# Kernel tuning notes

Hardware: AMD Instinct MI355X
Metric: run time of the kernel (lower is better)

The kernel has to match this reference:

```python
import jax, jax.numpy as jnp
import numpy as np

B, C, N = 32, 512, 1024   # batch, input channels, tokens
E, D, H = 512, 2048, 8    # d_input, d_model, heads
T, O = 50, 1000           # iterations, out_dims
NA, NO = 512, 512         # n_synch_action, n_synch_out


def setup_inputs() -> dict:
    key = jax.random.key(0)
    ks = jax.random.split(key, 16)
    s = 0.02
    rn = lambda k, shape: jax.random.normal(k, shape, jnp.float32) * s
    return dict(
        x=jax.random.normal(ks[0], (B, C, N), jnp.float32),
        W_kv=rn(ks[1], (C, E)), b_kv=jnp.zeros(E), g_kv=jnp.ones(E), be_kv=jnp.zeros(E),
        W_q=rn(ks[2], (NA, E)), b_q=jnp.zeros(E),
        W_in=rn(ks[3], (E, 3 * E)), b_in=jnp.zeros(3 * E),
        W_ao=rn(ks[4], (E, E)), b_ao=jnp.zeros(E),
        W_syn=rn(ks[5], (E + D, 2 * D)), b_syn=jnp.zeros(2 * D),
        g_syn=jnp.ones(D), be_syn=jnp.zeros(D),
        g_pm=jnp.ones(D), be_pm=jnp.zeros(D),
        W1=rn(ks[6], (D, D)), b1=jnp.zeros(D),
        W2=rn(ks[7], (D, D)), b2=jnp.zeros(D),
        start_state=jax.random.uniform(ks[8], (D,), jnp.float32, -0.1, 0.1),
        decay_action=jnp.zeros(NA), decay_out=jnp.zeros(NO),
        W_out=rn(ks[9], (NO, O)), b_out=jnp.zeros(O),
        idx_action=jax.random.permutation(ks[10], D)[:NA].astype(jnp.int32),
        idx_out=jax.random.permutation(ks[11], D)[:NO].astype(jnp.int32),
    )


def _ln(x, g, b, eps=1e-5):
    m = x.mean(-1, keepdims=True)
    v = ((x - m) ** 2).mean(-1, keepdims=True)
    return (x - m) * jax.lax.rsqrt(v + eps) * g + b


def reference(x, W_kv, b_kv, g_kv, be_kv, W_q, b_q, W_in, b_in, W_ao, b_ao,
              W_syn, b_syn, g_syn, be_syn, g_pm, be_pm, W1, b1, W2, b2,
              start_state, decay_action, decay_out, W_out, b_out,
              idx_action, idx_out):
    Bx = x.shape[0]
    hd = E // H
    # features: backbone='none', pos='none' -> flatten(2).transpose(1,2) then kv_proj
    feats = jnp.transpose(x, (0, 2, 1))                 # [B,N,C]
    kv = _ln(feats @ W_kv + b_kv, g_kv, be_kv)          # [B,N,E]
    # MHA K/V are constant across iterations -> hoist
    Wq_a, Wk_a, Wv_a = jnp.split(W_in, 3, axis=1)
    bq_a, bk_a, bv_a = jnp.split(b_in, 3)
    K = (kv @ Wk_a + bk_a).reshape(Bx, N, H, hd)
    V = (kv @ Wv_a + bv_a).reshape(Bx, N, H, hd)
    r_a = jnp.exp(-jnp.clip(decay_action, 0.0, 15.0))   # [NA]
    r_o = jnp.exp(-jnp.clip(decay_out, 0.0, 15.0))      # [NO]
    act0 = jnp.broadcast_to(start_state, (Bx, D))
    zA = jnp.zeros((Bx, NA), jnp.float32)
    zO = jnp.zeros((Bx, NO), jnp.float32)
    logO = jnp.log(jnp.float32(O))
    scale = 1.0 / jnp.sqrt(jnp.float32(hd))

    def step(carry, _):
        act, aA, bA, aO, bO = carry
        # action sync (left == right in the source, so products are squares)
        sel = act[:, idx_action]
        aA = r_a * aA + sel * sel
        bA = r_a * bA + 1.0
        syncA = aA * jax.lax.rsqrt(bA)                  # [B,NA]
        # cross-attention query
        q = syncA @ W_q + b_q                           # [B,E]
        qh = (q @ Wq_a + bq_a).reshape(Bx, H, hd)
        scores = jnp.einsum('bhd,bnhd->bhn', qh, K) * scale
        w = jax.nn.softmax(scores, axis=-1)
        attn = jnp.einsum('bhn,bnhd->bhd', w, V).reshape(Bx, E)
        attn = attn @ W_ao + b_ao
        # synapses: LazyLinear(2D) -> GLU -> LayerNorm (dropout=0)
        h = jnp.concatenate([attn, act], axis=-1) @ W_syn + b_syn
        a_half, g_half = jnp.split(h, 2, axis=-1)
        state = _ln(a_half * jax.nn.sigmoid(g_half), g_syn, be_syn)
        # post-synapse MLP: LN -> Linear -> ReLU -> Linear -> ReLU
        hpm = _ln(state, g_pm, be_pm)
        act = jax.nn.relu(jax.nn.relu(hpm @ W1 + b1) @ W2 + b2)
        # out sync
        selo = act[:, idx_out]
        aO = r_o * aO + selo * selo
        bO = r_o * bO + 1.0
        syncO = aO * jax.lax.rsqrt(bO)                  # [B,NO]
        pred = syncO @ W_out + b_out                    # [B,O]
        lp = jax.nn.log_softmax(pred, axis=-1)
        ne = -jnp.sum(jnp.exp(lp) * lp, axis=-1) / logO
        cert = jnp.stack([ne, 1.0 - ne], axis=-1)       # [B,2]
        return (act, aA, bA, aO, bO), (pred, cert, syncO)

    _, (preds, certs, syncs) = jax.lax.scan(step, (act0, zA, zA, zO, zO), None, length=T)
    predictions = jnp.transpose(preds, (1, 2, 0))       # [B,O,T]
    certainties = jnp.transpose(certs, (1, 2, 0))       # [B,2,T]
    return predictions, certainties, syncs[-1]
```

## Files before the change

kernel.cpp:

```cpp
#include <hip/hip_runtime.h>


typedef unsigned short u16;
typedef unsigned int uv4 __attribute__((ext_vector_type(4)));
typedef float fv4 __attribute__((ext_vector_type(4)));
typedef float fv2 __attribute__((ext_vector_type(2)));

__device__ __forceinline__ float bf2f(u16 u) {
    return __uint_as_float(((unsigned int)u) << 16);
}
__device__ __forceinline__ float bflo(unsigned int u) { return __uint_as_float(u << 16); }
__device__ __forceinline__ float bfhi(unsigned int u) { return __uint_as_float(u & 0xffff0000u); }
__device__ __forceinline__ u16 f2bf(float f) {
    unsigned int u = __float_as_uint(f);
    unsigned int r = u + 0x7fffu + ((u >> 16) & 1u);
    return (u16)(r >> 16);
}

__device__ __forceinline__ void cload(fv4& r, const void* p) {
    asm volatile("global_load_dwordx4 %0, %1, off sc0 sc1" : "=v"(r) : "v"(p));
}
__device__ __forceinline__ void cload2(fv2& r, const void* p) {
    asm volatile("global_load_dwordx2 %0, %1, off sc0 sc1" : "=v"(r) : "v"(p));
}
__device__ __forceinline__ void cstore4(void* p, fv4 v) {
    asm volatile("global_store_dwordx4 %0, %1, off sc0 sc1" :: "v"(p), "v"(v) : "memory");
}
__device__ __forceinline__ void cstore2(void* p, fv2 v) {
    asm volatile("global_store_dwordx2 %0, %1, off sc0 sc1" :: "v"(p), "v"(v) : "memory");
}
__device__ __forceinline__ void cwait1(fv4& a) {
    asm volatile("s_waitcnt vmcnt(0)" : "+v"(a) :: "memory");
    __builtin_amdgcn_sched_barrier(0);
}
__device__ __forceinline__ void cwait2(fv4& a, fv4& b) {
    asm volatile("s_waitcnt vmcnt(0)" : "+v"(a), "+v"(b) :: "memory");
    __builtin_amdgcn_sched_barrier(0);
}
__device__ __forceinline__ void cwaitf2(fv2& a) {
    asm volatile("s_waitcnt vmcnt(0)" : "+v"(a) :: "memory");
    __builtin_amdgcn_sched_barrier(0);
}

__device__ __forceinline__ float aload(const float* p) {
    return __hip_atomic_load((const float*)p, __ATOMIC_RELAXED, __HIP_MEMORY_SCOPE_AGENT);
}

__global__ __launch_bounds__(256) void k_init(
    const float* __restrict__ start_state, const float* __restrict__ dec_a,
    const float* __restrict__ dec_o,
    float* act0, float* aA, float* bA, float* aO, float* bO,
    float* r_a, float* r_o, unsigned* bar)
{
    int g = blockIdx.x * 256 + threadIdx.x;
    int T = gridDim.x * 256;
    for (int i = g; i < 32 * 2048; i += T) act0[i] = start_state[i & 2047];
    for (int i = g; i < 32 * 512; i += T) { aA[i] = 0.f; bA[i] = 0.f; aO[i] = 0.f; bO[i] = 0.f; }
    for (int i = g; i < 512; i += T) {
        float da = fminf(fmaxf(dec_a[i], 0.f), 15.f);
        float dv = fminf(fmaxf(dec_o[i], 0.f), 15.f);
        r_a[i] = __expf(-da);
        r_o[i] = __expf(-dv);
    }
    if (g < 2048) bar[g] = 0u;
}

__global__ __launch_bounds__(256) void k_gemm_xT(
    const float* __restrict__ x, const float* __restrict__ Wkv,
    const float* __restrict__ bkv, float* __restrict__ out)
{
    __shared__ float As[16 * 68];
    __shared__ float Bs[16 * 132];
    int tid = threadIdx.x;
    int tn = tid & 15, tm = tid >> 4;
    int n0 = blockIdx.x * 128;
    int r0 = blockIdx.y * 64;
    int b = r0 >> 10;
    int nrow0 = r0 & 1023;
    const float* xb = x + (size_t)b * 512 * 1024;
    float acc[4][8];
#pragma unroll
    for (int i = 0; i < 4; ++i)
#pragma unroll
        for (int j = 0; j < 8; ++j) acc[i][j] = 0.f;

    for (int k0 = 0; k0 < 512; k0 += 16) {
        __syncthreads();
#pragma unroll
        for (int l = 0; l < 4; ++l) {
            int i = tid + l * 256;
            int nn = i & 63, kk = i >> 6;
            As[kk * 68 + nn] = xb[(size_t)(k0 + kk) * 1024 + nrow0 + nn];
        }
#pragma unroll
        for (int l = 0; l < 8; ++l) {
            int i = tid + l * 256;
            int n = i & 127, kk = i >> 7;
            Bs[kk * 132 + n] = Wkv[(size_t)(k0 + kk) * 512 + n0 + n];
        }
        __syncthreads();
#pragma unroll
        for (int k = 0; k < 16; ++k) {
            float4 a4 = *(const float4*)&As[k * 68 + tm * 4];
            float4 b0 = *(const float4*)&Bs[k * 132 + tn * 8];
            float4 b1 = *(const float4*)&Bs[k * 132 + tn * 8 + 4];
            float av[4] = {a4.x, a4.y, a4.z, a4.w};
            float bv[8] = {b0.x, b0.y, b0.z, b0.w, b1.x, b1.y, b1.z, b1.w};
#pragma unroll
            for (int i = 0; i < 4; ++i)
#pragma unroll
                for (int j = 0; j < 8; ++j) acc[i][j] += av[i] * bv[j];
        }
    }
#pragma unroll
    for (int i = 0; i < 4; ++i) {
        int r = r0 + tm * 4 + i;
        int c = n0 + tn * 8;
        float* orow = out + (size_t)r * 512 + c;
#pragma unroll
        for (int j = 0; j < 8; ++j) orow[j] = acc[i][j] + bkv[c + j];
    }
}

__global__ __launch_bounds__(256) void k_gemm_AB(
    const float* __restrict__ A, int lda,
    const float* __restrict__ B, int ldb,
    const float* __restrict__ bias,
    u16* __restrict__ out, int N)
{
    __shared__ float As[16 * 68];
    __shared__ float Bs[16 * 132];
    int tid = threadIdx.x;
    int tn = tid & 15, tm = tid >> 4;
    int n0 = blockIdx.x * 128;
    int r0 = blockIdx.y * 64;
    float acc[4][8];
#pragma unroll
    for (int i = 0; i < 4; ++i)
#pragma unroll
        for (int j = 0; j < 8; ++j) acc[i][j] = 0.f;

    for (int k0 = 0; k0 < 512; k0 += 16) {
        __syncthreads();
#pragma unroll
        for (int l = 0; l < 4; ++l) {
            int i = tid + l * 256;
            int kk = i & 15, m = i >> 4;
            As[kk * 68 + m] = A[(size_t)(r0 + m) * lda + k0 + kk];
        }
#pragma unroll
        for (int l = 0; l < 8; ++l) {
            int i = tid + l * 256;
            int n = i & 127, kk = i >> 7;
            Bs[kk * 132 + n] = B[(size_t)(k0 + kk) * ldb + n0 + n];
        }
        __syncthreads();
#pragma unroll
        for (int k = 0; k < 16; ++k) {
            float4 a4 = *(const float4*)&As[k * 68 + tm * 4];
            float4 b0 = *(const float4*)&Bs[k * 132 + tn * 8];
            float4 b1 = *(const float4*)&Bs[k * 132 + tn * 8 + 4];
            float av[4] = {a4.x, a4.y, a4.z, a4.w};
            float bv[8] = {b0.x, b0.y, b0.z, b0.w, b1.x, b1.y, b1.z, b1.w};
#pragma unroll
            for (int i = 0; i < 4; ++i)
#pragma unroll
                for (int j = 0; j < 8; ++j) acc[i][j] += av[i] * bv[j];
        }
    }
#pragma unroll
    for (int i = 0; i < 4; ++i) {
        int r = r0 + tm * 4 + i;
        int c = n0 + tn * 8;
        float vv[8];
#pragma unroll
        for (int j = 0; j < 8; ++j) vv[j] = acc[i][j] + (bias ? bias[c + j] : 0.f);
        unsigned int w0 = (unsigned int)f2bf(vv[0]) | ((unsigned int)f2bf(vv[1]) << 16);
        unsigned int w1 = (unsigned int)f2bf(vv[2]) | ((unsigned int)f2bf(vv[3]) << 16);
        unsigned int w2 = (unsigned int)f2bf(vv[4]) | ((unsigned int)f2bf(vv[5]) << 16);
        unsigned int w3 = (unsigned int)f2bf(vv[6]) | ((unsigned int)f2bf(vv[7]) << 16);
        *(uint4*)&out[(size_t)r * N + c] = make_uint4(w0, w1, w2, w3);
    }
}

__global__ __launch_bounds__(256) void k_ln_kv(
    float* __restrict__ kv, const float* __restrict__ g, const float* __restrict__ be)
{
    int tid = threadIdx.x;
    int lane = tid & 63;
    int row = blockIdx.x * 4 + (tid >> 6);
    float* p = kv + (size_t)row * 512 + lane * 8;
    float4 u0 = *(float4*)p;
    float4 u1 = *(float4*)(p + 4);
    float v[8] = {u0.x, u0.y, u0.z, u0.w, u1.x, u1.y, u1.z, u1.w};
    float s = 0.f, s2 = 0.f;
#pragma unroll
    for (int i = 0; i < 8; ++i) { s += v[i]; s2 += v[i] * v[i]; }
#pragma unroll
    for (int off = 32; off >= 1; off >>= 1) {
        s += __shfl_xor(s, off, 64);
        s2 += __shfl_xor(s2, off, 64);
    }
    float m = s * (1.f / 512.f);
    float var = s2 * (1.f / 512.f) - m * m;
    float rs = rsqrtf(var + 1e-5f);
    const float* gp = g + lane * 8;
    const float* bp = be + lane * 8;
#pragma unroll
    for (int i = 0; i < 8; ++i) v[i] = (v[i] - m) * rs * gp[i] + bp[i];
    *(float4*)p = make_float4(v[0], v[1], v[2], v[3]);
    *(float4*)(p + 4) = make_float4(v[4], v[5], v[6], v[7]);
}

__global__ __launch_bounds__(256) void k_bvec(
    const float* __restrict__ vin, const float* __restrict__ B, int ldb,
    const float* __restrict__ badd, float* __restrict__ out, int Nj)
{
    int j = blockIdx.x * 256 + threadIdx.x;
    if (j >= Nj) return;
    float s = 0.f;
    for (int e = 0; e < 512; ++e) s += vin[e] * B[(size_t)e * ldb + j];
    out[j] = s + badd[j];
}

__global__ __launch_bounds__(256) void k_convert(
    const float* __restrict__ src, u16* __restrict__ dst, int n)
{
    int g = blockIdx.x * 256 + threadIdx.x;
    int T = gridDim.x * 256;
    for (int i = g; i < n; i += T) dst[i] = f2bf(src[i]);
}

__global__ __launch_bounds__(256) void k_transpose_wout(
    const float* __restrict__ W, u16* __restrict__ WT)
{
    int j = blockIdx.x * 256 + threadIdx.x;
    if (j >= 1000) return;
    for (int k = 0; k < 512; ++k) WT[(size_t)j * 512 + k] = f2bf(W[(size_t)k * 1000 + j]);
}

__global__ __launch_bounds__(256) void k_transpose_v(
    const u16* __restrict__ V, u16* __restrict__ VT)
{
    int bh = blockIdx.x;
    int b = bh >> 3, h = bh & 7;
    int tid = threadIdx.x;
    const u16* src = V + (size_t)b * 1024 * 512 + h * 64;
    u16* dst = VT + (size_t)bh * 64 * 1024;
    int n0 = tid * 4;
    for (int d = 0; d < 64; ++d) {
        u16 a0 = src[(size_t)(n0 + 0) * 512 + d];
        u16 a1 = src[(size_t)(n0 + 1) * 512 + d];
        u16 a2 = src[(size_t)(n0 + 2) * 512 + d];
        u16 a3 = src[(size_t)(n0 + 3) * 512 + d];
        uint2 w = make_uint2((unsigned)a0 | ((unsigned)a1 << 16),
                             (unsigned)a2 | ((unsigned)a3 << 16));
        *(uint2*)&dst[(size_t)d * 1024 + n0] = w;
    }
}

#define NBLK 1024

struct LoopP {
    const u16* Wqq; const float* bqq;
    const u16* K;   const u16* VT;
    const u16* Wfull; const float* bcomb;
    const u16* W1; const float* b1;
    const u16* W2; const float* b2;
    const u16* WoutT; const float* bout;
    const int* idxA; const int* idxO;
    const float* r_a; const float* r_o;
    float* aA0; float* aA1; float* bA0; float* bA1;
    float* aO0; float* aO1; float* bO0; float* bO1;
    float* act0; float* act1;
    float* pvp; float* mz;
    float* attn_f; float* actR;
    float* h_pre; float* hpm; float* t1;
    float* out;
    const float* gsyn; const float* besyn; const float* gpm; const float* bepm;
    unsigned* bar;
};

union Smem {
    struct { float sA[512]; float qh[64]; float sc[256]; float red[512]; } at;
    struct { float mzs[64]; float arow[512]; } b2;
    struct { float Al[32 * 36]; } sk;
    struct { float red[16]; } gl;
    struct { float sO[512]; float red[8]; } pr;
};

__device__ __forceinline__ void gridbar(unsigned* bar)
{
    __syncthreads();
    if (threadIdx.x == 0) {
        int blk = blockIdx.x;
        unsigned* cnt1 = bar + ((blk >> 6) << 5);
        unsigned* cnt2 = bar + (16 << 5);
        unsigned* genp = bar + ((17 + (blk & 31)) << 5);
        unsigned g = __hip_atomic_load(genp, __ATOMIC_RELAXED, __HIP_MEMORY_SCOPE_AGENT);
        asm volatile("s_waitcnt vmcnt(0)" ::: "memory");
        unsigned a = __hip_atomic_fetch_add(cnt1, 1u, __ATOMIC_RELAXED, __HIP_MEMORY_SCOPE_AGENT);
        if (a == 63u) {
            __hip_atomic_store(cnt1, 0u, __ATOMIC_RELAXED, __HIP_MEMORY_SCOPE_AGENT);
            asm volatile("s_waitcnt vmcnt(0)" ::: "memory");
            unsigned a2 = __hip_atomic_fetch_add(cnt2, 1u, __ATOMIC_RELAXED, __HIP_MEMORY_SCOPE_AGENT);
            if (a2 == 15u) {
                __hip_atomic_store(cnt2, 0u, __ATOMIC_RELAXED, __HIP_MEMORY_SCOPE_AGENT);
                asm volatile("s_waitcnt vmcnt(0)" ::: "memory");
#pragma unroll
                for (int r = 0; r < 32; ++r)
                    __hip_atomic_store(bar + ((17 + r) << 5), g + 1u,
                                       __ATOMIC_RELAXED, __HIP_MEMORY_SCOPE_AGENT);
            }
        }
        unsigned cur;
        do {
            cur = __hip_atomic_load(genp, __ATOMIC_RELAXED, __HIP_MEMORY_SCOPE_AGENT);
            if (cur != g) break;
            __builtin_amdgcn_s_sleep(2);
        } while (true);
        asm volatile("" ::: "memory");
    }
    __syncthreads();
}

__device__ __forceinline__ void red2(float& a, float& b, float* red, int tid)
{
#pragma unroll
    for (int off = 32; off >= 1; off >>= 1) {
        a += __shfl_xor(a, off, 64);
        b += __shfl_xor(b, off, 64);
    }
    __syncthreads();
    if ((tid & 63) == 0) { red[(tid >> 6) * 2] = a; red[(tid >> 6) * 2 + 1] = b; }
    __syncthreads();
    float sa = 0.f, sb = 0.f;
#pragma unroll
    for (int w = 0; w < 8; ++w) { sa += red[2 * w]; sb += red[2 * w + 1]; }
    a = sa; b = sb;
}

__global__ __launch_bounds__(512, 8) void k_loop(LoopP P)
{
    __shared__ Smem s;
    const int tid = threadIdx.x;
    const int blk = blockIdx.x;
    const int lane = tid & 63;
    const int wav = tid >> 6;

    for (int t = 0; t < 50; ++t) {
        const float* actprev = (t & 1) ? P.act1 : P.act0;
        float*       actnext = (t & 1) ? P.act0 : P.act1;
        const float* aAp = (t & 1) ? P.aA1 : P.aA0;  float* aAc = (t & 1) ? P.aA0 : P.aA1;
        const float* bAp = (t & 1) ? P.bA1 : P.bA0;  float* bAc = (t & 1) ? P.bA0 : P.bA1;
        const float* aOp = (t & 1) ? P.aO1 : P.aO0;  float* aOc = (t & 1) ? P.aO0 : P.aO1;
        const float* bOp = (t & 1) ? P.bO1 : P.bO0;  float* bOc = (t & 1) ? P.bO0 : P.bO1;

        __syncthreads();

        {
            int bh = blk >> 2, p = blk & 3;
            int b = bh >> 3, h = bh & 7;
            if (tid < 64) {
                int g4 = blk * 64 + tid;
                fv4 zz = {0.f, 0.f, 0.f, 0.f};
                if (g4 < 32768) cstore4(&P.h_pre[g4 * 4], zz);
                else if (g4 < 49152) cstore4(&P.t1[(g4 - 32768) * 4], zz);
                else cstore4(&actnext[(g4 - 49152) * 4], zz);
            }
            if (p == 0 && tid >= 64 && tid < 128) {
                int i4 = (h * 64 + (tid - 64)) * 4;
                fv4 v;
                cload(v, &actprev[b * 2048 + i4]);
                cwait1(v);
                if (t > 0) {
                    float4 b4 = *(const float4*)&P.b2[i4];
                    v.x = fmaxf(0.f, v.x + b4.x);
                    v.y = fmaxf(0.f, v.y + b4.y);
                    v.z = fmaxf(0.f, v.z + b4.z);
                    v.w = fmaxf(0.f, v.w + b4.w);
                }
                cstore4(&P.actR[b * 2048 + i4], v);
            }
            {
                int j = tid;
                int ia = P.idxA[j];
                float v = aload(&actprev[b * 2048 + ia]);
                if (t > 0) v = fmaxf(0.f, v + P.b2[ia]);
                float r = P.r_a[j];
                float a = r * aAp[b * 512 + j] + v * v;
                float bb = r * bAp[b * 512 + j] + 1.f;
                aAc[b * 512 + j] = a; bAc[b * 512 + j] = bb;
                s.at.sA[j] = a * rsqrtf(bb);
            }
            __syncthreads();
            {
                int d = tid & 63, kg = tid >> 6;
                const u16* wp = P.Wqq + (size_t)(kg * 64) * 512 + h * 64 + d;
                const float* ap = s.at.sA + kg * 64;
                float pq = 0.f;
#pragma unroll 16
                for (int k = 0; k < 64; ++k) pq += ap[k] * bf2f(wp[(size_t)k * 512]);
                s.at.red[tid] = pq;
            }
            __syncthreads();
            if (tid < 64) {
                float q = P.bqq[h * 64 + tid];
#pragma unroll
                for (int g2 = 0; g2 < 8; ++g2) q += s.at.red[g2 * 64 + tid];
                s.at.qh[tid] = q;
            }
            __syncthreads();
            if (tid < 256) {
                const u16* Kbh = P.K + (size_t)b * 1024 * 512 + h * 64;
                const uv4* kp = (const uv4*)(Kbh + (size_t)(p * 256 + tid) * 512);
                uv4 u[8];
#pragma unroll
                for (int i = 0; i < 8; ++i) u[i] = __builtin_nontemporal_load(kp + i);
                float dot = 0.f;
#pragma unroll
                for (int i = 0; i < 8; ++i) {
                    float4 q0 = *(float4*)&s.at.qh[i * 8];
                    float4 q1 = *(float4*)&s.at.qh[i * 8 + 4];
                    dot += q0.x * bflo(u[i].x) + q0.y * bfhi(u[i].x)
                         + q0.z * bflo(u[i].y) + q0.w * bfhi(u[i].y)
                         + q1.x * bflo(u[i].z) + q1.y * bfhi(u[i].z)
                         + q1.z * bflo(u[i].w) + q1.w * bfhi(u[i].w);
                }
                s.at.sc[tid] = dot * 0.125f;
            }
            __syncthreads();
            float mv = (tid < 256) ? s.at.sc[tid] : -1e30f;
#pragma unroll
            for (int off = 32; off >= 1; off >>= 1) mv = fmaxf(mv, __shfl_xor(mv, off, 64));
            if (lane == 0) s.at.red[wav] = mv;
            __syncthreads();
            float mloc = s.at.red[0];
#pragma unroll
            for (int w = 1; w < 8; ++w) mloc = fmaxf(mloc, s.at.red[w]);
            float ev = 0.f;
            if (tid < 256) {
                ev = __expf(s.at.sc[tid] - mloc);
                s.at.sc[tid] = ev;
            }
            float zv = ev;
#pragma unroll
            for (int off = 32; off >= 1; off >>= 1) zv += __shfl_xor(zv, off, 64);
            __syncthreads();
            if (lane == 0) s.at.red[wav] = zv;
            __syncthreads();
            float Zloc = 0.f;
#pragma unroll
            for (int w = 0; w < 8; ++w) Zloc += s.at.red[w];
            __syncthreads();
            {
                int d = tid & 63, ng = tid >> 6;
                const uv4* vp = (const uv4*)(P.VT
                    + ((size_t)bh * 64 + d) * 1024 + p * 256 + ng * 32);
                float acc = 0.f;
#pragma unroll
                for (int i = 0; i < 4; ++i) {
                    uv4 u = __builtin_nontemporal_load(vp + i);
                    const float* so = s.at.sc + ng * 32 + i * 8;
                    acc += so[0] * bflo(u.x) + so[1] * bfhi(u.x)
                         + so[2] * bflo(u.y) + so[3] * bfhi(u.y)
                         + so[4] * bflo(u.z) + so[5] * bfhi(u.z)
                         + so[6] * bflo(u.w) + so[7] * bfhi(u.w);
                }
                s.at.red[tid] = acc;
            }
            __syncthreads();
            if (tid < 64) {
                float a = 0.f;
#pragma unroll
                for (int g2 = 0; g2 < 8; ++g2) a += s.at.red[g2 * 64 + tid];
                s.at.qh[tid] = a;
            }
            __syncthreads();
            if (tid < 16) {
                fv4 v = *(fv4*)&s.at.qh[tid * 4];
                cstore4(&P.pvp[((size_t)p * 256 + bh) * 64 + tid * 4], v);
            }
            if (tid == 0) {
                fv2 v; v.x = mloc; v.y = Zloc;
                cstore2(&P.mz[(p * 256 + bh) * 2], v);
            }
        }
        gridbar(P.bar);

        if (blk < 32) {
            int b = blk;
            if (tid < 32) {
                int p = tid >> 3, h = tid & 7;
                fv2 v;
                cload2(v, &P.mz[(p * 256 + b * 8 + h) * 2]);
                cwaitf2(v);
                s.b2.mzs[tid * 2] = v.x;
                s.b2.mzs[tid * 2 + 1] = v.y;
            }
            __syncthreads();
            int h = tid >> 6, d = tid & 63;
            int rh = b * 8 + h;
            float m0 = s.b2.mzs[(0 * 8 + h) * 2], z0 = s.b2.mzs[(0 * 8 + h) * 2 + 1];
            float m1 = s.b2.mzs[(1 * 8 + h) * 2], z1 = s.b2.mzs[(1 * 8 + h) * 2 + 1];
            float m2 = s.b2.mzs[(2 * 8 + h) * 2], z2 = s.b2.mzs[(2 * 8 + h) * 2 + 1];
            float m3 = s.b2.mzs[(3 * 8 + h) * 2], z3 = s.b2.mzs[(3 * 8 + h) * 2 + 1];
            float M = fmaxf(fmaxf(m0, m1), fmaxf(m2, m3));
            float e0 = __expf(m0 - M), e1 = __expf(m1 - M);
            float e2 = __expf(m2 - M), e3 = __expf(m3 - M);
            float Zinv = 1.f / (z0 * e0 + z1 * e1 + z2 * e2 + z3 * e3);
            float acc = aload(&P.pvp[((size_t)0 * 256 + rh) * 64 + d]) * e0
                      + aload(&P.pvp[((size_t)1 * 256 + rh) * 64 + d]) * e1
                      + aload(&P.pvp[((size_t)2 * 256 + rh) * 64 + d]) * e2
                      + aload(&P.pvp[((size_t)3 * 256 + rh) * 64 + d]) * e3;
            s.b2.arow[tid] = acc * Zinv;
            __syncthreads();
            if (tid < 128) {
                fv4 v = *(fv4*)&s.b2.arow[tid * 4];
                cstore4(&P.attn_f[b * 512 + tid * 4], v);
            }
        }
        gridbar(P.bar);

        {
            int kb = blk >> 6, jb = blk & 63;
            int j = jb * 64 + (tid & 63);
            int rg = tid >> 6;
            int kbeg = kb * 160;
            float a0 = 0.f, a1 = 0.f, a2 = 0.f, a3 = 0.f;
            for (int k0 = kbeg; k0 < kbeg + 160; k0 += 32) {
                __syncthreads();
                if (tid < 256) {
                    int k4 = (tid & 7) * 4, r = tid >> 3;
                    int kk = k0 + k4;
                    fv4 v;
                    if (kk < 512) {
                        cload(v, &P.attn_f[r * 512 + kk]);
                        cwait1(v);
                    } else {
                        cload(v, &P.actR[r * 2048 + kk - 512]);
                        cwait1(v);
                    }
                    s.sk.Al[(k4 + 0) * 36 + r] = v.x;
                    s.sk.Al[(k4 + 1) * 36 + r] = v.y;
                    s.sk.Al[(k4 + 2) * 36 + r] = v.z;
                    s.sk.Al[(k4 + 3) * 36 + r] = v.w;
                }
                __syncthreads();
                const u16* wp = P.Wfull + (size_t)k0 * 4096 + j;
#pragma unroll 32
                for (int k = 0; k < 32; ++k) {
                    float w = bf2f(wp[(size_t)k * 4096]);
                    float4 a = *(const float4*)&s.sk.Al[k * 36 + rg * 4];
                    a0 += a.x * w; a1 += a.y * w; a2 += a.z * w; a3 += a.w * w;
                }
            }
            int r0 = rg * 4;
            atomicAdd(&P.h_pre[(size_t)(r0 + 0) * 4096 + j], a0);
            atomicAdd(&P.h_pre[(size_t)(r0 + 1) * 4096 + j], a1);
            atomicAdd(&P.h_pre[(size_t)(r0 + 2) * 4096 + j], a2);
            atomicAdd(&P.h_pre[(size_t)(r0 + 3) * 4096 + j], a3);
        }
        gridbar(P.bar);

        if (blk < 32) {
            const float* hr = P.h_pre + (size_t)blk * 4096;
            int i4 = tid * 4;
            fv4 av, gv;
            cload(av, hr + i4);
            cload(gv, hr + 2048 + i4);
            cwait2(av, gv);
            float4 bc1 = *(const float4*)&P.bcomb[i4];
            float4 bc2 = *(const float4*)&P.bcomb[2048 + i4];
            fv4 z;
            z.x = (av.x + bc1.x) / (1.f + __expf(-(gv.x + bc2.x)));
            z.y = (av.y + bc1.y) / (1.f + __expf(-(gv.y + bc2.y)));
            z.z = (av.z + bc1.z) / (1.f + __expf(-(gv.z + bc2.z)));
            z.w = (av.w + bc1.w) / (1.f + __expf(-(gv.w + bc2.w)));
            float sa = z.x + z.y + z.z + z.w;
            float sb = z.x * z.x + z.y * z.y + z.z * z.z + z.w * z.w;
            red2(sa, sb, s.gl.red, tid);
            float m1 = sa * (1.f / 2048.f);
            float v1 = sb * (1.f / 2048.f) - m1 * m1;
            float rs1 = rsqrtf(v1 + 1e-5f);
            float4 gs = *(const float4*)&P.gsyn[i4];
            float4 bs = *(const float4*)&P.besyn[i4];
            z.x = (z.x - m1) * rs1 * gs.x + bs.x;
            z.y = (z.y - m1) * rs1 * gs.y + bs.y;
            z.z = (z.z - m1) * rs1 * gs.z + bs.z;
            z.w = (z.w - m1) * rs1 * gs.w + bs.w;
            float ta = z.x + z.y + z.z + z.w;
            float tb = z.x * z.x + z.y * z.y + z.z * z.z + z.w * z.w;
            red2(ta, tb, s.gl.red, tid);
            float m2 = ta * (1.f / 2048.f);
            float v2 = tb * (1.f / 2048.f) - m2 * m2;
            float rs2 = rsqrtf(v2 + 1e-5f);
            float4 gp = *(const float4*)&P.gpm[i4];
            float4 bp = *(const float4*)&P.bepm[i4];
            fv4 o;
            o.x = (z.x - m2) * rs2 * gp.x + bp.x;
            o.y = (z.y - m2) * rs2 * gp.y + bp.y;
            o.z = (z.z - m2) * rs2 * gp.z + bp.z;
            o.w = (z.w - m2) * rs2 * gp.w + bp.w;
            cstore4(&P.hpm[(size_t)blk * 2048 + i4], o);
        }
        gridbar(P.bar);

        {
            int kb = blk >> 5, jb = blk & 31;
            int j = jb * 64 + (tid & 63);
            int rg = tid >> 6;
            int kbeg = kb * 64;
            float a0 = 0.f, a1 = 0.f, a2 = 0.f, a3 = 0.f;
            for (int k0 = kbeg; k0 < kbeg + 64; k0 += 32) {
                __syncthreads();
                if (tid < 256) {
                    int k4 = (tid & 7) * 4, r = tid >> 3;
                    fv4 v;
                    cload(v, &P.hpm[r * 2048 + k0 + k4]);
                    cwait1(v);
                    s.sk.Al[(k4 + 0) * 36 + r] = v.x;
                    s.sk.Al[(k4 + 1) * 36 + r] = v.y;
                    s.sk.Al[(k4 + 2) * 36 + r] = v.z;
                    s.sk.Al[(k4 + 3) * 36 + r] = v.w;
                }
                __syncthreads();
                const u16* wp = P.W1 + (size_t)k0 * 2048 + j;
#pragma unroll 32
                for (int k = 0; k < 32; ++k) {
                    float w = bf2f(wp[(size_t)k * 2048]);
                    float4 a = *(const float4*)&s.sk.Al[k * 36 + rg * 4];
                    a0 += a.x * w; a1 += a.y * w; a2 += a.z * w; a3 += a.w * w;
                }
            }
            int r0 = rg * 4;
            atomicAdd(&P.t1[(r0 + 0) * 2048 + j], a0);
            atomicAdd(&P.t1[(r0 + 1) * 2048 + j], a1);
            atomicAdd(&P.t1[(r0 + 2) * 2048 + j], a2);
            atomicAdd(&P.t1[(r0 + 3) * 2048 + j], a3);
        }
        gridbar(P.bar);

        {
            int kb = blk >> 5, jb = blk & 31;
            int j = jb * 64 + (tid & 63);
            int rg = tid >> 6;
            int kbeg = kb * 64;
            float a0 = 0.f, a1 = 0.f, a2 = 0.f, a3 = 0.f;
            for (int k0 = kbeg; k0 < kbeg + 64; k0 += 32) {
                __syncthreads();
                if (tid < 256) {
                    int k4 = (tid & 7) * 4, r = tid >> 3;
                    int kk = k0 + k4;
                    fv4 v;
                    cload(v, &P.t1[r * 2048 + kk]);
                    cwait1(v);
                    float4 b4 = *(const float4*)&P.b1[kk];
                    s.sk.Al[(k4 + 0) * 36 + r] = fmaxf(0.f, v.x + b4.x);
                    s.sk.Al[(k4 + 1) * 36 + r] = fmaxf(0.f, v.y + b4.y);
                    s.sk.Al[(k4 + 2) * 36 + r] = fmaxf(0.f, v.z + b4.z);
                    s.sk.Al[(k4 + 3) * 36 + r] = fmaxf(0.f, v.w + b4.w);
                }
                __syncthreads();
                const u16* wp = P.W2 + (size_t)k0 * 2048 + j;
#pragma unroll 32
                for (int k = 0; k < 32; ++k) {
                    float w = bf2f(wp[(size_t)k * 2048]);
                    float4 a = *(const float4*)&s.sk.Al[k * 36 + rg * 4];
                    a0 += a.x * w; a1 += a.y * w; a2 += a.z * w; a3 += a.w * w;
                }
            }
            int r0 = rg * 4;
            atomicAdd(&actnext[(r0 + 0) * 2048 + j], a0);
            atomicAdd(&actnext[(r0 + 1) * 2048 + j], a1);
            atomicAdd(&actnext[(r0 + 2) * 2048 + j], a2);
            atomicAdd(&actnext[(r0 + 3) * 2048 + j], a3);
        }
        gridbar(P.bar);

        if (blk < 32) {
            int b = blk;
            {
                int j2 = tid;
                int io = P.idxO[j2];
                float v = fmaxf(0.f, aload(&actnext[b * 2048 + io]) + P.b2[io]);
                float r = P.r_o[j2];
                float a = r * aOp[b * 512 + j2] + v * v;
                float bb = r * bOp[b * 512 + j2] + 1.f;
                aOc[b * 512 + j2] = a; bOc[b * 512 + j2] = bb;
                float sy = a * rsqrtf(bb);
                s.pr.sO[j2] = sy;
                if (t == 49) P.out[1603200 + b * 512 + j2] = sy;
            }
            __syncthreads();
            bool has1 = tid < 488;
            float p0, p1 = -1e30f;
            {
                const uint4* wp = (const uint4*)(P.WoutT + (size_t)tid * 512);
                float acc = 0.f;
#pragma unroll 16
                for (int i = 0; i < 64; ++i) {
                    uint4 u = wp[i];
                    const float* so = s.pr.sO + i * 8;
                    acc += so[0] * bflo(u.x) + so[1] * bfhi(u.x)
                         + so[2] * bflo(u.y) + so[3] * bfhi(u.y)
                         + so[4] * bflo(u.z) + so[5] * bfhi(u.z)
                         + so[6] * bflo(u.w) + so[7] * bfhi(u.w);
                }
                p0 = acc + P.bout[tid];
            }
            if (has1) {
                const uint4* wp = (const uint4*)(P.WoutT + (size_t)(tid + 512) * 512);
                float acc = 0.f;
#pragma unroll 16
                for (int i = 0; i < 64; ++i) {
                    uint4 u = wp[i];
                    const float* so = s.pr.sO + i * 8;
                    acc += so[0] * bflo(u.x) + so[1] * bfhi(u.x)
                         + so[2] * bflo(u.y) + so[3] * bfhi(u.y)
                         + so[4] * bflo(u.z) + so[5] * bfhi(u.z)
                         + so[6] * bflo(u.w) + so[7] * bfhi(u.w);
                }
                p1 = acc + P.bout[tid + 512];
            }
            float mx = fmaxf(p0, p1);
#pragma unroll
            for (int off = 32; off >= 1; off >>= 1) mx = fmaxf(mx, __shfl_xor(mx, off, 64));
            __syncthreads();
            if (lane == 0) s.pr.red[wav] = mx;
            __syncthreads();
            mx = s.pr.red[0];
#pragma unroll
            for (int w = 1; w < 8; ++w) mx = fmaxf(mx, s.pr.red[w]);
            float zs = __expf(p0 - mx) + (has1 ? __expf(p1 - mx) : 0.f);
#pragma unroll
            for (int off = 32; off >= 1; off >>= 1) zs += __shfl_xor(zs, off, 64);
            __syncthreads();
            if (lane == 0) s.pr.red[wav] = zs;
            __syncthreads();
            float Z = 0.f;
#pragma unroll
            for (int w = 0; w < 8; ++w) Z += s.pr.red[w];
            float logZ = __logf(Z);
            float lp0 = p0 - mx - logZ;
            float se = __expf(lp0) * lp0;
            if (has1) { float lp1 = p1 - mx - logZ; se += __expf(lp1) * lp1; }
#pragma unroll
            for (int off = 32; off >= 1; off >>= 1) se += __shfl_xor(se, off, 64);
            __syncthreads();
            if (lane == 0) s.pr.red[wav] = se;
            __syncthreads();
            float S = 0.f;
#pragma unroll
            for (int w = 0; w < 8; ++w) S += s.pr.red[w];
            float ne = -S / logf(1000.0f);
            P.out[(size_t)b * 50000 + (size_t)tid * 50 + t] = p0;
            if (has1) P.out[(size_t)b * 50000 + (size_t)(tid + 512) * 50 + t] = p1;
            if (tid == 0) {
                P.out[1600000 + b * 100 + t] = ne;
                P.out[1600000 + b * 100 + 50 + t] = 1.f - ne;
            }
        }
    }
}

extern "C" void kernel_launch(void* const* d_in, const int* in_sizes, int n_in,
                              void* d_out, int out_size, void* d_ws, size_t ws_size,
                              hipStream_t stream)
{
    const float* x      = (const float*)d_in[0];
    const float* W_kv   = (const float*)d_in[1];
    const float* b_kv   = (const float*)d_in[2];
    const float* g_kv   = (const float*)d_in[3];
    const float* be_kv  = (const float*)d_in[4];
    const float* W_q    = (const float*)d_in[5];
    const float* b_q    = (const float*)d_in[6];
    const float* W_in   = (const float*)d_in[7];
    const float* b_in   = (const float*)d_in[8];
    const float* W_ao   = (const float*)d_in[9];
    const float* b_ao   = (const float*)d_in[10];
    const float* W_syn  = (const float*)d_in[11];
    const float* b_syn  = (const float*)d_in[12];
    const float* g_syn  = (const float*)d_in[13];
    const float* be_syn = (const float*)d_in[14];
    const float* g_pm   = (const float*)d_in[15];
    const float* be_pm  = (const float*)d_in[16];
    const float* W1     = (const float*)d_in[17];
    const float* b1     = (const float*)d_in[18];
    const float* W2     = (const float*)d_in[19];
    const float* b2     = (const float*)d_in[20];
    const float* start_state  = (const float*)d_in[21];
    const float* decay_action = (const float*)d_in[22];
    const float* decay_out    = (const float*)d_in[23];
    const float* W_out  = (const float*)d_in[24];
    const float* b_out  = (const float*)d_in[25];
    const int* idx_action = (const int*)d_in[26];
    const int* idx_out    = (const int*)d_in[27];
    float* out = (float*)d_out;

    char* ws = (char*)d_ws;
    size_t off = 0;
    auto take = [&](size_t bytes) -> char* {
        char* p = ws + off;
        off += (bytes + 255) & ~(size_t)255;
        return p;
    };

    char* region0 = take(67108864);
    float* kv = (float*)region0;
    u16* W_full = (u16*)region0;
    u16* W1b    = (u16*)(region0 + 20971520);
    u16* W2b    = (u16*)(region0 + 29360128);
    u16* WoutT  = (u16*)(region0 + 37748736);
    u16* Wqqb   = (u16*)(region0 + 38772736);

    u16* K_bf = (u16*)take(33554432);
    u16* V_bf = (u16*)take(33554432);
    u16* V_T  = (u16*)take(33554432);
    float* b_qq   = (float*)take(2048);
    float* b_comb = (float*)take(16384);
    float* r_a = (float*)take(2048);
    float* r_o = (float*)take(2048);
    float* aA0 = (float*)take(65536);
    float* aA1 = (float*)take(65536);
    float* bA0 = (float*)take(65536);
    float* bA1 = (float*)take(65536);
    float* aO0 = (float*)take(65536);
    float* aO1 = (float*)take(65536);
    float* bO0 = (float*)take(65536);
    float* bO1 = (float*)take(65536);
    float* act0v = (float*)take(262144);
    float* act1v = (float*)take(262144);
    float* h_pre = (float*)take(524288);
    float* hpm   = (float*)take(262144);
    float* t1_pre = (float*)take(262144);
    float* pvp = (float*)take(262144);
    float* mzB = (float*)take(8192);
    float* attn_f = (float*)take(65536);
    float* actR   = (float*)take(262144);
    unsigned* bar = (unsigned*)take(8192);
    (void)ws_size; (void)in_sizes; (void)n_in; (void)out_size;

    k_init<<<256, 256, 0, stream>>>(start_state, decay_action, decay_out,
                                    act0v, aA0, bA0, aO0, bO0, r_a, r_o, bar);
    k_gemm_xT<<<dim3(4, 512), 256, 0, stream>>>(x, W_kv, b_kv, kv);
    k_ln_kv<<<8192, 256, 0, stream>>>(kv, g_kv, be_kv);
    k_gemm_AB<<<dim3(4, 512), 256, 0, stream>>>(kv, 512, W_in + 512, 1536, b_in + 512, K_bf, 512);
    k_gemm_AB<<<dim3(4, 512), 256, 0, stream>>>(kv, 512, W_in + 1024, 1536, b_in + 1024, V_bf, 512);
    k_transpose_v<<<256, 256, 0, stream>>>(V_bf, V_T);
    k_gemm_AB<<<dim3(4, 8), 256, 0, stream>>>(W_q, 512, W_in, 1536, nullptr, Wqqb, 512);
    k_gemm_AB<<<dim3(32, 8), 256, 0, stream>>>(W_ao, 512, W_syn, 4096, nullptr, W_full, 4096);
    k_bvec<<<2, 256, 0, stream>>>(b_q, W_in, 1536, b_in, b_qq, 512);
    k_bvec<<<16, 256, 0, stream>>>(b_ao, W_syn, 4096, b_syn, b_comb, 4096);
    k_convert<<<2048, 256, 0, stream>>>(W_syn + (size_t)512 * 4096, W_full + (size_t)512 * 4096, 2048 * 4096);
    k_convert<<<2048, 256, 0, stream>>>(W1, W1b, 2048 * 2048);
    k_convert<<<2048, 256, 0, stream>>>(W2, W2b, 2048 * 2048);
    k_transpose_wout<<<4, 256, 0, stream>>>(W_out, WoutT);

    LoopP p;
    p.Wqq = Wqqb; p.bqq = b_qq;
    p.K = K_bf;   p.VT = V_T;
    p.Wfull = W_full; p.bcomb = b_comb;
    p.W1 = W1b; p.b1 = b1;
    p.W2 = W2b; p.b2 = b2;
    p.WoutT = WoutT; p.bout = b_out;
    p.idxA = idx_action; p.idxO = idx_out;
    p.r_a = r_a; p.r_o = r_o;
    p.aA0 = aA0; p.aA1 = aA1; p.bA0 = bA0; p.bA1 = bA1;
    p.aO0 = aO0; p.aO1 = aO1; p.bO0 = bO0; p.bO1 = bO1;
    p.act0 = act0v; p.act1 = act1v;
    p.pvp = pvp; p.mz = mzB;
    p.attn_f = attn_f; p.actR = actR;
    p.h_pre = h_pre; p.hpm = hpm; p.t1 = t1_pre;
    p.out = out;
    p.gsyn = g_syn; p.besyn = be_syn; p.gpm = g_pm; p.bepm = be_pm;
    p.bar = bar;

    k_loop<<<dim3(NBLK), dim3(512), 0, stream>>>(p);
}
```

Baseline: 10.32 ms.

## Retile K, V and loop weight matrices into per-block contiguous tiles

Adds preprocessing kernels that rearrange K into per-(batch,head) contiguous rows, V into per-block transposed chunks, and the synapse, W1 and W2 bf16 weights into contiguous per-(jb,kb) tiles. Inside the persistent loop kernel, each block's slice then sits in one contiguous region, which improves DRAM locality and cache-line use for the weight streams read every iteration. The cost is extra one-time retile kernels and reusing the K/V scratch buffers as weight tile storage.

```diff
diff --git a/kernel.cpp b/kernel.cpp
--- a/kernel.cpp
+++ b/kernel.cpp
@@ -239,23 +239,56 @@
     for (int k = 0; k < 512; ++k) WT[(size_t)j * 512 + k] = f2bf(W[(size_t)k * 1000 + j]);
 }
 
-__global__ __launch_bounds__(256) void k_transpose_v(
-    const u16* __restrict__ V, u16* __restrict__ VT)
+__global__ __launch_bounds__(256) void k_retile_K(
+    const u16* __restrict__ K, u16* __restrict__ Kr)
 {
     int bh = blockIdx.x;
     int b = bh >> 3, h = bh & 7;
     int tid = threadIdx.x;
-    const u16* src = V + (size_t)b * 1024 * 512 + h * 64;
-    u16* dst = VT + (size_t)bh * 64 * 1024;
-    int n0 = tid * 4;
-    for (int d = 0; d < 64; ++d) {
-        u16 a0 = src[(size_t)(n0 + 0) * 512 + d];
-        u16 a1 = src[(size_t)(n0 + 1) * 512 + d];
-        u16 a2 = src[(size_t)(n0 + 2) * 512 + d];
-        u16 a3 = src[(size_t)(n0 + 3) * 512 + d];
-        uint2 w = make_uint2((unsigned)a0 | ((unsigned)a1 << 16),
-                             (unsigned)a2 | ((unsigned)a3 << 16));
-        *(uint2*)&dst[(size_t)d * 1024 + n0] = w;
+    for (int n = tid; n < 1024; n += 256) {
+        const uv4* src = (const uv4*)(K + (size_t)(b * 1024 + n) * 512 + h * 64);
+        uv4* dst = (uv4*)(Kr + ((size_t)bh * 1024 + n) * 64);
+#pragma unroll
+        for (int i = 0; i < 8; ++i) dst[i] = src[i];
+    }
+}
+
+__global__ __launch_bounds__(256) void k_retile_V(
+    const u16* __restrict__ V, u16* __restrict__ VTp)
+{
+    int blk = blockIdx.x;
+    int bh = blk >> 2, p = blk & 3;
+    int b = bh >> 3, h = bh & 7;
+    int tid = threadIdx.x;
+    int d = tid & 63, q = tid >> 6;
+    u16 buf[64];
+    for (int i = 0; i < 64; ++i)
+        buf[i] = V[(size_t)(b * 1024 + p * 256 + q * 64 + i) * 512 + h * 64 + d];
+    u16* dst = VTp + ((size_t)blk * 64 + d) * 256 + q * 64;
+    for (int i = 0; i < 16; ++i) ((uv4*)dst)[i] = ((uv4*)buf)[i];
+}
+
+__global__ __launch_bounds__(256) void k_retile_WC(
+    const u16* __restrict__ W, u16* __restrict__ WT)
+{
+    int tau = blockIdx.x;
+    int jb = tau >> 4, kb = tau & 15;
+    int tid = threadIdx.x;
+    for (int m = tid; m < 160 * 64; m += 256) {
+        int kk = m >> 6, jj = m & 63;
+        WT[(size_t)tau * 10240 + m] = W[(size_t)(kb * 160 + kk) * 4096 + jb * 64 + jj];
+    }
+}
+
+__global__ __launch_bounds__(256) void k_retile_W64(
+    const u16* __restrict__ W, u16* __restrict__ WT)
+{
+    int tau = blockIdx.x;
+    int jb = tau >> 5, kb = tau & 31;
+    int tid = threadIdx.x;
+    for (int m = tid; m < 64 * 64; m += 256) {
+        int kk = m >> 6, jj = m & 63;
+        WT[(size_t)tau * 4096 + m] = W[(size_t)(kb * 64 + kk) * 2048 + jb * 64 + jj];
     }
 }
 
@@ -263,10 +296,10 @@
 
 struct LoopP {
     const u16* Wqq; const float* bqq;
-    const u16* K;   const u16* VT;
-    const u16* Wfull; const float* bcomb;
-    const u16* W1; const float* b1;
-    const u16* W2; const float* b2;
+    const u16* Kr;  const u16* VTp;
+    const u16* WCt; const float* bcomb;
+    const u16* W1t; const float* b1;
+    const u16* W2t; const float* b2;
     const u16* WoutT; const float* bout;
     const int* idxA; const int* idxO;
     const float* r_a; const float* r_o;
@@ -412,8 +445,8 @@
             }
             __syncthreads();
             if (tid < 256) {
-                const u16* Kbh = P.K + (size_t)b * 1024 * 512 + h * 64;
-                const uv4* kp = (const uv4*)(Kbh + (size_t)(p * 256 + tid) * 512);
+                const uv4* kp = (const uv4*)(P.Kr
+                    + ((size_t)bh * 1024 + p * 256 + tid) * 64);
                 uv4 u[8];
 #pragma unroll
                 for (int i = 0; i < 8; ++i) u[i] = __builtin_nontemporal_load(kp + i);
@@ -455,8 +488,8 @@
             __syncthreads();
             {
                 int d = tid & 63, ng = tid >> 6;
-                const uv4* vp = (const uv4*)(P.VT
-                    + ((size_t)bh * 64 + d) * 1024 + p * 256 + ng * 32);
+                const uv4* vp = (const uv4*)(P.VTp
+                    + ((size_t)blk * 64 + d) * 256 + ng * 32);
                 float acc = 0.f;
 #pragma unroll
                 for (int i = 0; i < 4; ++i) {
@@ -527,6 +560,7 @@
             int j = jb * 64 + (tid & 63);
             int rg = tid >> 6;
             int kbeg = kb * 160;
+            const u16* wtile = P.WCt + (size_t)(jb * 16 + kb) * 10240;
             float a0 = 0.f, a1 = 0.f, a2 = 0.f, a3 = 0.f;
             for (int k0 = kbeg; k0 < kbeg + 160; k0 += 32) {
                 __syncthreads();
@@ -547,10 +581,10 @@
                     s.sk.Al[(k4 + 3) * 36 + r] = v.w;
                 }
                 __syncthreads();
-                const u16* wp = P.Wfull + (size_t)k0 * 4096 + j;
+                const u16* wp = wtile + (size_t)(k0 - kbeg) * 64 + (tid & 63);
 #pragma unroll 32
                 for (int k = 0; k < 32; ++k) {
-                    float w = bf2f(wp[(size_t)k * 4096]);
+                    float w = bf2f(wp[k * 64]);
                     float4 a = *(const float4*)&s.sk.Al[k * 36 + rg * 4];
                     a0 += a.x * w; a1 += a.y * w; a2 += a.z * w; a3 += a.w * w;
                 }
@@ -611,6 +645,7 @@
             int j = jb * 64 + (tid & 63);
             int rg = tid >> 6;
             int kbeg = kb * 64;
+            const u16* wtile = P.W1t + (size_t)(jb * 32 + kb) * 4096;
             float a0 = 0.f, a1 = 0.f, a2 = 0.f, a3 = 0.f;
             for (int k0 = kbeg; k0 < kbeg + 64; k0 += 32) {
                 __syncthreads();
@@ -625,10 +660,10 @@
                     s.sk.Al[(k4 + 3) * 36 + r] = v.w;
                 }
                 __syncthreads();
-                const u16* wp = P.W1 + (size_t)k0 * 2048 + j;
+                const u16* wp = wtile + (size_t)(k0 - kbeg) * 64 + (tid & 63);
 #pragma unroll 32
                 for (int k = 0; k < 32; ++k) {
-                    float w = bf2f(wp[(size_t)k * 2048]);
+                    float w = bf2f(wp[k * 64]);
                     float4 a = *(const float4*)&s.sk.Al[k * 36 + rg * 4];
                     a0 += a.x * w; a1 += a.y * w; a2 += a.z * w; a3 += a.w * w;
                 }
@@ -646,6 +681,7 @@
             int j = jb * 64 + (tid & 63);
             int rg = tid >> 6;
             int kbeg = kb * 64;
+            const u16* wtile = P.W2t + (size_t)(jb * 32 + kb) * 4096;
             float a0 = 0.f, a1 = 0.f, a2 = 0.f, a3 = 0.f;
             for (int k0 = kbeg; k0 < kbeg + 64; k0 += 32) {
                 __syncthreads();
@@ -662,10 +698,10 @@
                     s.sk.Al[(k4 + 3) * 36 + r] = fmaxf(0.f, v.w + b4.w);
                 }
                 __syncthreads();
-                const u16* wp = P.W2 + (size_t)k0 * 2048 + j;
+                const u16* wp = wtile + (size_t)(k0 - kbeg) * 64 + (tid & 63);
 #pragma unroll 32
                 for (int k = 0; k < 32; ++k) {
-                    float w = bf2f(wp[(size_t)k * 2048]);
+                    float w = bf2f(wp[k * 64]);
                     float4 a = *(const float4*)&s.sk.Al[k * 36 + rg * 4];
                     a0 += a.x * w; a1 += a.y * w; a2 += a.z * w; a3 += a.w * w;
                 }
@@ -816,7 +852,11 @@
 
     u16* K_bf = (u16*)take(33554432);
     u16* V_bf = (u16*)take(33554432);
-    u16* V_T  = (u16*)take(33554432);
+    u16* K_r  = (u16*)take(33554432);
+    u16* VT_p = (u16*)take(33554432);
+    u16* WT_C = K_bf;
+    u16* WT_1 = V_bf;
+    u16* WT_2 = V_bf + 4194304;
     float* b_qq   = (float*)take(2048);
     float* b_comb = (float*)take(16384);
     float* r_a = (float*)take(2048);
@@ -847,7 +887,8 @@
     k_ln_kv<<<8192, 256, 0, stream>>>(kv, g_kv, be_kv);
     k_gemm_AB<<<dim3(4, 512), 256, 0, stream>>>(kv, 512, W_in + 512, 1536, b_in + 512, K_bf, 512);
     k_gemm_AB<<<dim3(4, 512), 256, 0, stream>>>(kv, 512, W_in + 1024, 1536, b_in + 1024, V_bf, 512);
-    k_transpose_v<<<256, 256, 0, stream>>>(V_bf, V_T);
+    k_retile_K<<<256, 256, 0, stream>>>(K_bf, K_r);
+    k_retile_V<<<1024, 256, 0, stream>>>(V_bf, VT_p);
     k_gemm_AB<<<dim3(4, 8), 256, 0, stream>>>(W_q, 512, W_in, 1536, nullptr, Wqqb, 512);
     k_gemm_AB<<<dim3(32, 8), 256, 0, stream>>>(W_ao, 512, W_syn, 4096, nullptr, W_full, 4096);
     k_bvec<<<2, 256, 0, stream>>>(b_q, W_in, 1536, b_in, b_qq, 512);
@@ -856,13 +897,16 @@
     k_convert<<<2048, 256, 0, stream>>>(W1, W1b, 2048 * 2048);
     k_convert<<<2048, 256, 0, stream>>>(W2, W2b, 2048 * 2048);
     k_transpose_wout<<<4, 256, 0, stream>>>(W_out, WoutT);
+    k_retile_WC<<<1024, 256, 0, stream>>>(W_full, WT_C);
+    k_retile_W64<<<1024, 256, 0, stream>>>(W1b, WT_1);
+    k_retile_W64<<<1024, 256, 0, stream>>>(W2b, WT_2);
 
     LoopP p;
     p.Wqq = Wqqb; p.bqq = b_qq;
-    p.K = K_bf;   p.VT = V_T;
-    p.Wfull = W_full; p.bcomb = b_comb;
-    p.W1 = W1b; p.b1 = b1;
-    p.W2 = W2b; p.b2 = b2;
+    p.Kr = K_r;   p.VTp = VT_p;
+    p.WCt = WT_C; p.bcomb = b_comb;
+    p.W1t = WT_1; p.b1 = b1;
+    p.W2t = WT_2; p.b2 = b2;
     p.WoutT = WoutT; p.bout = b_out;
     p.idxA = idx_action; p.idxO = idx_out;
     p.r_a = r_a; p.r_o = r_o;
```

After: 10.33 ms. No clear change (+0.0%).
